# Performance work log

Measured on AMD Instinct MI355X. Metric: run time of the kernel, lower is better.

## Reference

```python
import jax, jax.numpy as jnp
import numpy as np

ATTRIBUTE_NUMS = [3, 3, 1, 4, 3]
WINDOW_SIZE = 10


def setup_inputs() -> dict:
    key = jax.random.key(0)
    ks = jax.random.split(key, 7)
    b, s, n_l, f = 4, 2048, 4, 64
    A, L = 14, 5  # num_attributes, levels per attribute
    scale_tensor = jax.random.normal(ks[0], (b, s, n_l, f), dtype=jnp.float32)
    scale = 1.0 / np.sqrt(f).astype(np.float32)
    Wq = jax.random.normal(ks[1], (A, L, f, f), dtype=jnp.float32) * scale
    bq = jax.random.normal(ks[2], (A, L, f), dtype=jnp.float32) * 0.01
    Wk = jax.random.normal(ks[3], (A, L, f, f), dtype=jnp.float32) * scale
    bk = jax.random.normal(ks[4], (A, L, f), dtype=jnp.float32) * 0.01
    Wt = jax.random.normal(ks[5], (A, L, f, f), dtype=jnp.float32) * scale
    bt = jax.random.normal(ks[6], (A, L, f), dtype=jnp.float32) * 0.01
    return {"scale_tensor": scale_tensor, "Wq": Wq, "bq": bq, "Wk": Wk,
            "bk": bk, "Wt": Wt, "bt": bt, "scale_idx": 4}


def reference(scale_tensor, Wq, bq, Wk, bk, Wt, bt, scale_idx):
    b, s, a, f = scale_tensor.shape
    k = WINDOW_SIZE * (6 - scale_idx)  # half window (static python int)
    w = 2 * k + 1
    l_i = scale_idx
    off = sum(ATTRIBUTE_NUMS[:scale_idx - 1])
    # select the parameters actually used: attributes [off, off+a), levels [0, l_i)
    Wq_s, bq_s = Wq[off:off + a, :l_i], bq[off:off + a, :l_i]  # [a,l,f,f], [a,l,f]
    Wk_s, bk_s = Wk[off:off + a, :l_i], bk[off:off + a, :l_i]
    Wt_s, bt_s = Wt[off:off + a, :l_i], bt[off:off + a, :l_i]

    # sliding windows over the sequence axis (zero-padded), shared across levels
    padded = jnp.pad(scale_tensor, ((0, 0), (k, k), (0, 0), (0, 0)))
    idx = jnp.arange(s)[:, None] + jnp.arange(w)[None, :]  # [s, w]
    win = padded[:, idx]                                   # [b,s,w,a,f]
    zero_mask = jnp.all(win == 0, axis=-1)                 # [b,s,w,a]

    # queries: q = x @ Wq^T + bq  (torch Linear convention, W is [out,in])
    q = jnp.einsum('bsaf,algf->bsalg', scale_tensor, Wq_s) + bq_s  # [b,s,a,l,f]
    qk = jnp.einsum('bsalg,algf->bsalf', q, Wk_s)                  # [b,s,a,l,f]
    attn = jnp.einsum('bsalf,bswaf->bsalw', qk, win)
    attn = attn + jnp.einsum('bsalg,alg->bsal', q, bk_s)[..., None]
    attn = attn / np.float32(np.sqrt(f))

    mask = jnp.transpose(zero_mask, (0, 1, 3, 2))[:, :, :, None, :]  # [b,s,a,1,w]
    attn = jnp.where(mask, jnp.float32(-1e9), attn)
    wgt = jax.nn.softmax(attn, axis=-1)                    # [b,s,a,l,w]

    ctx = jnp.einsum('bsalw,bswaf->bsalf', wgt, win)       # [b,s,a,l,f]
    out = jnp.einsum('bsalf,algf->bsalg', ctx, Wt_s) + bt_s
    return out  # [b,s,a,l_i,f]
```

## Files before the change

kernel.cpp:

```cpp
#include <hip/hip_runtime.h>
#include <hip/hip_bf16.h>

#define SDIM 2048
#define KWIN 20
#define WWIN 41

typedef __attribute__((ext_vector_type(8))) short s8v;
typedef __attribute__((ext_vector_type(4))) float f32x4;
#define MFMA __builtin_amdgcn_mfma_f32_16x16x32_bf16

#define WSB_MB 8256
#define WSB_WT 172096

#define O_YJF 0
#define O_YFJ 16128
#define O_RF  31488
#define LDS_TOTAL 31936

__device__ __forceinline__ int detect_is_bf16(const void* xp) {
  const unsigned* w = (const unsigned*)xp;
  const unsigned word = w[threadIdx.x & 63];
  const unsigned e = (word >> 7) & 0xFFu;
  const unsigned long long m = __ballot(e >= 118u && e <= 132u);
  return __popcll(m) >= 32;
}
__device__ __forceinline__ float ldf(const void* p, size_t i, int isbf) {
  return isbf ? __bfloat162float(((const __hip_bfloat16*)p)[i]) : ((const float*)p)[i];
}
__device__ __forceinline__ unsigned bfb(float f) {
  union { float f; unsigned u; } x; x.f = f;
  return (x.u + 0x7FFFu + ((x.u >> 16) & 1u)) >> 16;
}
__device__ __forceinline__ int pkbf(float a, float b) {
  return (int)(bfb(a) | (bfb(b) << 16));
}
__device__ __forceinline__ s8v xform(int p00, int p01, int p10, int p11, int lane) {
  const int q = lane >> 4;
  const int sA = (lane & 15) + ((q & 1) << 5);
  const int sB = sA + 16;
  const bool hi = (q >> 1) != 0;
  const int w0a = __shfl(p00, sA), w0b = __shfl(p10, sA);
  const int w1a = __shfl(p01, sA), w1b = __shfl(p11, sA);
  const int w2a = __shfl(p00, sB), w2b = __shfl(p10, sB);
  const int w3a = __shfl(p01, sB), w3b = __shfl(p11, sB);
  union { int i[4]; s8v v; } u;
  u.i[0] = hi ? w0b : w0a;
  u.i[1] = hi ? w1b : w1a;
  u.i[2] = hi ? w2b : w2a;
  u.i[3] = hi ? w3b : w3a;
  return u.v;
}

__global__ __launch_bounds__(256) void prep_kernel(
    const void* __restrict__ x,
    const void* __restrict__ Wq, const void* __restrict__ bq,
    const void* __restrict__ Wk, const void* __restrict__ bk,
    const void* __restrict__ Wt, const void* __restrict__ bt,
    const int* __restrict__ sip, float* __restrict__ ws) {
  const int isbf = detect_is_bf16(x);
  const int al = blockIdx.x, a = al >> 2, li = al & 3;
  const int fq = blockIdx.y;
  const int si = *sip;
  int off = 0;
  const int ATTR[5] = {3, 3, 1, 4, 3};
  for (int i = 0; i < si - 1 && i < 5; ++i) off += ATTR[i];
  const size_t wb = ((size_t)(off + a) * 5 + li) * 4096;
  const size_t bb = ((size_t)(off + a) * 5 + li) * 64;
  const int tid = threadIdx.x;

  __shared__ float sq[4096], sk[4096];
  __shared__ float sbq[64], sbk[64];
  for (int i = tid; i < 4096; i += 256) {
    sq[i] = ldf(Wq, wb + i, isbf);
    sk[i] = ldf(Wk, wb + i, isbf);
  }
  if (tid < 64) { sbq[tid] = ldf(bq, bb + tid, isbf); sbk[tid] = ldf(bk, bb + tid, isbf); }
  __syncthreads();

  __hip_bfloat16* mb  = (__hip_bfloat16*)((char*)ws + WSB_MB) + (size_t)al * 5120;
  __hip_bfloat16* wtb = (__hip_bfloat16*)((char*)ws + WSB_WT) + (size_t)al * 4096;

  for (int t = tid; t < 1024; t += 256) {
    const int f = fq * 16 + (t >> 6), f2 = t & 63;
    float acc = 0.f;
    #pragma unroll 16
    for (int g = 0; g < 64; ++g) acc += sk[g * 64 + f] * sq[g * 64 + f2];
    mb[f * 64 + f2] = __float2bfloat16(acc);
    wtb[f * 64 + f2] = __float2bfloat16(ldf(Wt, wb + f * 64 + f2, isbf));
  }
  if (fq == 0) {
    if (tid < 64) {
      float u = 0.f, v = 0.f;
      for (int g = 0; g < 64; ++g) {
        u += sq[g * 64 + tid] * sbk[g];
        v += sk[g * 64 + tid] * sbq[g];
      }
      mb[64 * 64 + tid] = __float2bfloat16(u);
      ws[al * 64 + tid] = v;
      ws[1024 + al * 64 + tid] = ldf(bt, bb + tid, isbf);
    }
    for (int i = tid; i < 15 * 64; i += 256) mb[65 * 64 + i] = __float2bfloat16(0.f);
    if (tid == 0) {
      float c = 0.f;
      for (int g = 0; g < 64; ++g) c += sbq[g] * sbk[g];
      ws[2048 + al] = c;
    }
  }
}

__global__ __launch_bounds__(256, 4) void attn_kernel(
    const void* __restrict__ x, const float* __restrict__ ws,
    float* __restrict__ out) {
  const int isbf = detect_is_bf16(x);
  const int chunk = blockIdx.x;
  const int ba = blockIdx.y;
  const int lp = blockIdx.z;
  const int b = ba >> 2, a = ba & 3;
  const int s0 = chunk * 64;
  const int tid = threadIdx.x;
  const int lane = tid & 63;
  const int mt = tid >> 6;
  const int c16 = lane & 15;
  const int q = lane >> 4;

  __shared__ __align__(16) char lds[LDS_TOTAL];

  #pragma unroll
  for (int it = 0; it < 7; ++it) {
    const int r = it * 16 + (tid >> 4);
    const int j = s0 - KWIN + r;
    float4 yv = {0.f, 0.f, 0.f, 0.f};
    if (r < 104 && j >= 0 && j < SDIM) {
      if (isbf) {
        const size_t base = (((size_t)b * SDIM + j) * 4 + a) * 64 + c16 * 4;
        yv.x = ldf(x, base, 1); yv.y = ldf(x, base + 1, 1);
        yv.z = ldf(x, base + 2, 1); yv.w = ldf(x, base + 3, 1);
      } else {
        yv = *((const float4*)x + (((size_t)b * SDIM + j) * 4 + a) * 16 + c16);
      }
    }
    const int f0 = c16 * 4;
    ((int*)(lds + O_YJF + r * 144 + f0 * 2))[0] = pkbf(yv.x, yv.y);
    ((int*)(lds + O_YJF + r * 144 + f0 * 2))[1] = pkbf(yv.z, yv.w);
    *(unsigned short*)(lds + O_YFJ + (f0 + 0) * 240 + r * 2) = (unsigned short)bfb(yv.x);
    *(unsigned short*)(lds + O_YFJ + (f0 + 1) * 240 + r * 2) = (unsigned short)bfb(yv.y);
    *(unsigned short*)(lds + O_YFJ + (f0 + 2) * 240 + r * 2) = (unsigned short)bfb(yv.z);
    *(unsigned short*)(lds + O_YFJ + (f0 + 3) * 240 + r * 2) = (unsigned short)bfb(yv.w);
    const bool nz = (yv.x != 0.f) || (yv.y != 0.f) || (yv.z != 0.f) || (yv.w != 0.f);
    const unsigned long long m = __ballot(nz);
    if (c16 == 0) ((float*)(lds + O_RF))[r] = ((m >> (q * 16)) & 0xFFFFull) ? 1.f : 0.f;
  }
  __syncthreads();

  const short* mbase  = (const short*)((const char*)ws + WSB_MB);
  const short* wtbase = (const short*)((const char*)ws + WSB_WT);
  const char* yjf = lds + O_YJF;
  const char* yfj = lds + O_YFJ;

  const s8v xb0 = *(const s8v*)(yjf + (KWIN + 16 * mt + c16) * 144 + 16 * q);
  const s8v xb1 = *(const s8v*)(yjf + (KWIN + 16 * mt + c16) * 144 + 64 + 16 * q);
  float rfarr[16];
  #pragma unroll
  for (int nt = 0; nt < 4; ++nt) {
    const float4 t = *(const float4*)((const float*)(lds + O_RF) + 16 * mt + 16 * nt + 4 * q);
    rfarr[nt * 4 + 0] = t.x; rfarr[nt * 4 + 1] = t.y;
    rfarr[nt * 4 + 2] = t.z; rfarr[nt * 4 + 3] = t.w;
  }

  for (int li = 0; li < 2; ++li) {
    const int l = lp * 2 + li;
    const int al = a * 4 + l;
    const short* mb  = mbase + (size_t)al * 5120;
    const short* wtb = wtbase + (size_t)al * 4096;
    const float c_al = ws[2048 + al];

    int pq[4][2];
    f32x4 uacc = {0.f, 0.f, 0.f, 0.f};
    #pragma unroll
    for (int nt = 0; nt < 5; ++nt) {
      const int rowm = (nt < 4) ? (16 * nt + c16) : (64 + c16);
      const s8v a0 = *(const s8v*)(mb + rowm * 64 + 8 * q);
      const s8v a1 = *(const s8v*)(mb + rowm * 64 + 32 + 8 * q);
      f32x4 acc;
      if (nt < 4) {
        const float4 v4 = *(const float4*)(ws + al * 64 + 16 * nt + 4 * q);
        acc[0] = v4.x; acc[1] = v4.y; acc[2] = v4.z; acc[3] = v4.w;
      } else {
        acc[0] = acc[1] = acc[2] = acc[3] = 0.f;
      }
      acc = MFMA(a0, xb0, acc, 0, 0, 0);
      acc = MFMA(a1, xb1, acc, 0, 0, 0);
      if (nt < 4) { pq[nt][0] = pkbf(acc[0], acc[1]); pq[nt][1] = pkbf(acc[2], acc[3]); }
      else uacc = acc;
    }
    const float ux = __shfl(uacc[0], lane & 15) + c_al;
    const s8v qb0 = xform(pq[0][0], pq[0][1], pq[1][0], pq[1][1], lane);
    const s8v qb1 = xform(pq[2][0], pq[2][1], pq[3][0], pq[3][1], lane);

    f32x4 st[4];
    #pragma unroll
    for (int nt = 0; nt < 4; ++nt) {
      const char* yr = yjf + (16 * mt + 16 * nt + c16) * 144 + 16 * q;
      const s8v a0 = *(const s8v*)yr;
      const s8v a1 = *(const s8v*)(yr + 64);
      f32x4 s = {0.f, 0.f, 0.f, 0.f};
      s = MFMA(a0, qb0, s, 0, 0, 0);
      s = MFMA(a1, qb1, s, 0, 0, 0);
      st[nt] = s;
    }

    float ee[16];
    float mx = -3.0e38f;
    #pragma unroll
    for (int nt = 0; nt < 4; ++nt)
      #pragma unroll
      for (int r = 0; r < 4; ++r) {
        const int w = 16 * nt + 4 * q + r - c16;
        float lv = -1.0e9f;
        if (w >= 0 && w < WWIN && rfarr[nt * 4 + r] != 0.f)
          lv = (st[nt][r] + ux) * 0.125f;
        ee[nt * 4 + r] = lv;
        mx = fmaxf(mx, lv);
      }
    mx = fmaxf(mx, __shfl_xor(mx, 16));
    mx = fmaxf(mx, __shfl_xor(mx, 32));
    float se = 0.f;
    #pragma unroll
    for (int i = 0; i < 16; ++i) { ee[i] = __expf(ee[i] - mx); se += ee[i]; }
    se += __shfl_xor(se, 16);
    se += __shfl_xor(se, 32);
    const float rse = 1.f / se;

    int pp[4][2];
    #pragma unroll
    for (int nt = 0; nt < 4; ++nt) {
      pp[nt][0] = pkbf(ee[nt * 4 + 0], ee[nt * 4 + 1]);
      pp[nt][1] = pkbf(ee[nt * 4 + 2], ee[nt * 4 + 3]);
    }
    const s8v pb0 = xform(pp[0][0], pp[0][1], pp[1][0], pp[1][1], lane);
    const s8v pb1 = xform(pp[2][0], pp[2][1], pp[3][0], pp[3][1], lane);

    int cp[4][2];
    #pragma unroll
    for (int nt = 0; nt < 4; ++nt) {
      const char* fr = yfj + (16 * nt + c16) * 240 + 32 * mt + 16 * q;
      const s8v a0 = *(const s8v*)fr;
      const s8v a1 = *(const s8v*)(fr + 64);
      f32x4 cc = {0.f, 0.f, 0.f, 0.f};
      cc = MFMA(a0, pb0, cc, 0, 0, 0);
      cc = MFMA(a1, pb1, cc, 0, 0, 0);
      cp[nt][0] = pkbf(cc[0] * rse, cc[1] * rse);
      cp[nt][1] = pkbf(cc[2] * rse, cc[3] * rse);
    }
    const s8v cb0 = xform(cp[0][0], cp[0][1], cp[1][0], cp[1][1], lane);
    const s8v cb1 = xform(cp[2][0], cp[2][1], cp[3][0], cp[3][1], lane);

    const int row = 16 * mt + c16;
    float* obase = out + ((((size_t)b * SDIM + s0 + row) * 4 + a) * 4 + l) * 64 + 4 * q;
    #pragma unroll
    for (int nt = 0; nt < 4; ++nt) {
      const s8v a0 = *(const s8v*)(wtb + (16 * nt + c16) * 64 + 8 * q);
      const s8v a1 = *(const s8v*)(wtb + (16 * nt + c16) * 64 + 32 + 8 * q);
      const float4 b4 = *(const float4*)(ws + 1024 + al * 64 + 16 * nt + 4 * q);
      f32x4 o;
      o[0] = b4.x; o[1] = b4.y; o[2] = b4.z; o[3] = b4.w;
      o = MFMA(a0, cb0, o, 0, 0, 0);
      o = MFMA(a1, cb1, o, 0, 0, 0);
      float4 o4; o4.x = o[0]; o4.y = o[1]; o4.z = o[2]; o4.w = o[3];
      *(float4*)(obase + 16 * nt) = o4;
    }
  }
}

extern "C" void kernel_launch(void* const* d_in, const int* in_sizes, int n_in,
                              void* d_out, int out_size, void* d_ws, size_t ws_size,
                              hipStream_t stream) {
  const void* x  = d_in[0];
  const void* Wq = d_in[1];
  const void* bq = d_in[2];
  const void* Wk = d_in[3];
  const void* bk = d_in[4];
  const void* Wt = d_in[5];
  const void* bt = d_in[6];
  const int* sip = (const int*)d_in[7];
  float* ws = (float*)d_ws;
  float* out = (float*)d_out;

  prep_kernel<<<dim3(16, 4), 256, 0, stream>>>(x, Wq, bq, Wk, bk, Wt, bt, sip, ws);
  attn_kernel<<<dim3(32, 16, 2), 256, 0, stream>>>(x, ws, out);
}
```

Before: 118.7 us.

## Drop transposed LDS window copy and give each block a single level

Removes the second, transposed bf16 copy of the window tile from shared memory. The context MFMA operands are now gathered with eight strided 16-bit LDS reads from the row-major tile, which roughly halves LDS use per block. The grid doubles along z so each block handles one level instead of looping over two, and the occupancy hint in the launch bounds is dropped. The cost is that every block restages the window tile, doing twice the global loads and conversions in total, and the scalar strided LDS gathers may hit bank conflicts and add instructions.

```diff
diff --git a/kernel.cpp b/kernel.cpp
--- a/kernel.cpp
+++ b/kernel.cpp
@@ -13,9 +13,8 @@
 #define WSB_WT 172096
 
 #define O_YJF 0
-#define O_YFJ 16128
-#define O_RF  31488
-#define LDS_TOTAL 31936
+#define O_RF  16128
+#define LDS_TOTAL 16576
 
 __device__ __forceinline__ int detect_is_bf16(const void* xp) {
   const unsigned* w = (const unsigned*)xp;
@@ -108,13 +107,13 @@
   }
 }
 
-__global__ __launch_bounds__(256, 4) void attn_kernel(
+__global__ __launch_bounds__(256) void attn_kernel(
     const void* __restrict__ x, const float* __restrict__ ws,
     float* __restrict__ out) {
   const int isbf = detect_is_bf16(x);
   const int chunk = blockIdx.x;
   const int ba = blockIdx.y;
-  const int lp = blockIdx.z;
+  const int l = blockIdx.z;
   const int b = ba >> 2, a = ba & 3;
   const int s0 = chunk * 64;
   const int tid = threadIdx.x;
@@ -142,20 +141,17 @@
     const int f0 = c16 * 4;
     ((int*)(lds + O_YJF + r * 144 + f0 * 2))[0] = pkbf(yv.x, yv.y);
     ((int*)(lds + O_YJF + r * 144 + f0 * 2))[1] = pkbf(yv.z, yv.w);
-    *(unsigned short*)(lds + O_YFJ + (f0 + 0) * 240 + r * 2) = (unsigned short)bfb(yv.x);
-    *(unsigned short*)(lds + O_YFJ + (f0 + 1) * 240 + r * 2) = (unsigned short)bfb(yv.y);
-    *(unsigned short*)(lds + O_YFJ + (f0 + 2) * 240 + r * 2) = (unsigned short)bfb(yv.z);
-    *(unsigned short*)(lds + O_YFJ + (f0 + 3) * 240 + r * 2) = (unsigned short)bfb(yv.w);
     const bool nz = (yv.x != 0.f) || (yv.y != 0.f) || (yv.z != 0.f) || (yv.w != 0.f);
     const unsigned long long m = __ballot(nz);
     if (c16 == 0) ((float*)(lds + O_RF))[r] = ((m >> (q * 16)) & 0xFFFFull) ? 1.f : 0.f;
   }
   __syncthreads();
 
-  const short* mbase  = (const short*)((const char*)ws + WSB_MB);
-  const short* wtbase = (const short*)((const char*)ws + WSB_WT);
   const char* yjf = lds + O_YJF;
-  const char* yfj = lds + O_YFJ;
+  const int al = a * 4 + l;
+  const short* mb  = (const short*)((const char*)ws + WSB_MB) + (size_t)al * 5120;
+  const short* wtb = (const short*)((const char*)ws + WSB_WT) + (size_t)al * 4096;
+  const float c_al = ws[2048 + al];
 
   const s8v xb0 = *(const s8v*)(yjf + (KWIN + 16 * mt + c16) * 144 + 16 * q);
   const s8v xb1 = *(const s8v*)(yjf + (KWIN + 16 * mt + c16) * 144 + 64 + 16 * q);
@@ -167,108 +163,104 @@
     rfarr[nt * 4 + 2] = t.z; rfarr[nt * 4 + 3] = t.w;
   }
 
-  for (int li = 0; li < 2; ++li) {
-    const int l = lp * 2 + li;
-    const int al = a * 4 + l;
-    const short* mb  = mbase + (size_t)al * 5120;
-    const short* wtb = wtbase + (size_t)al * 4096;
-    const float c_al = ws[2048 + al];
-
-    int pq[4][2];
-    f32x4 uacc = {0.f, 0.f, 0.f, 0.f};
+  int pq[4][2];
+  f32x4 uacc = {0.f, 0.f, 0.f, 0.f};
+  #pragma unroll
+  for (int nt = 0; nt < 5; ++nt) {
+    const int rowm = (nt < 4) ? (16 * nt + c16) : (64 + c16);
+    const s8v a0 = *(const s8v*)(mb + rowm * 64 + 8 * q);
+    const s8v a1 = *(const s8v*)(mb + rowm * 64 + 32 + 8 * q);
+    f32x4 acc;
+    if (nt < 4) {
+      const float4 v4 = *(const float4*)(ws + al * 64 + 16 * nt + 4 * q);
+      acc[0] = v4.x; acc[1] = v4.y; acc[2] = v4.z; acc[3] = v4.w;
+    } else {
+      acc[0] = acc[1] = acc[2] = acc[3] = 0.f;
+    }
+    acc = MFMA(a0, xb0, acc, 0, 0, 0);
+    acc = MFMA(a1, xb1, acc, 0, 0, 0);
+    if (nt < 4) { pq[nt][0] = pkbf(acc[0], acc[1]); pq[nt][1] = pkbf(acc[2], acc[3]); }
+    else uacc = acc;
+  }
+  const float ux = __shfl(uacc[0], lane & 15) + c_al;
+  const s8v qb0 = xform(pq[0][0], pq[0][1], pq[1][0], pq[1][1], lane);
+  const s8v qb1 = xform(pq[2][0], pq[2][1], pq[3][0], pq[3][1], lane);
+
+  f32x4 st[4];
+  #pragma unroll
+  for (int nt = 0; nt < 4; ++nt) {
+    const char* yr = yjf + (16 * mt + 16 * nt + c16) * 144 + 16 * q;
+    const s8v a0 = *(const s8v*)yr;
+    const s8v a1 = *(const s8v*)(yr + 64);
+    f32x4 s = {0.f, 0.f, 0.f, 0.f};
+    s = MFMA(a0, qb0, s, 0, 0, 0);
+    s = MFMA(a1, qb1, s, 0, 0, 0);
+    st[nt] = s;
+  }
+
+  float ee[16];
+  float mx = -3.0e38f;
+  #pragma unroll
+  for (int nt = 0; nt < 4; ++nt)
     #pragma unroll
-    for (int nt = 0; nt < 5; ++nt) {
-      const int rowm = (nt < 4) ? (16 * nt + c16) : (64 + c16);
-      const s8v a0 = *(const s8v*)(mb + rowm * 64 + 8 * q);
-      const s8v a1 = *(const s8v*)(mb + rowm * 64 + 32 + 8 * q);
-      f32x4 acc;
-      if (nt < 4) {
-        const float4 v4 = *(const float4*)(ws + al * 64 + 16 * nt + 4 * q);
-        acc[0] = v4.x; acc[1] = v4.y; acc[2] = v4.z; acc[3] = v4.w;
-      } else {
-        acc[0] = acc[1] = acc[2] = acc[3] = 0.f;
-      }
-      acc = MFMA(a0, xb0, acc, 0, 0, 0);
-      acc = MFMA(a1, xb1, acc, 0, 0, 0);
-      if (nt < 4) { pq[nt][0] = pkbf(acc[0], acc[1]); pq[nt][1] = pkbf(acc[2], acc[3]); }
-      else uacc = acc;
-    }
-    const float ux = __shfl(uacc[0], lane & 15) + c_al;
-    const s8v qb0 = xform(pq[0][0], pq[0][1], pq[1][0], pq[1][1], lane);
-    const s8v qb1 = xform(pq[2][0], pq[2][1], pq[3][0], pq[3][1], lane);
-
-    f32x4 st[4];
+    for (int r = 0; r < 4; ++r) {
+      const int w = 16 * nt + 4 * q + r - c16;
+      float lv = -1.0e9f;
+      if (w >= 0 && w < WWIN && rfarr[nt * 4 + r] != 0.f)
+        lv = (st[nt][r] + ux) * 0.125f;
+      ee[nt * 4 + r] = lv;
+      mx = fmaxf(mx, lv);
+    }
+  mx = fmaxf(mx, __shfl_xor(mx, 16));
+  mx = fmaxf(mx, __shfl_xor(mx, 32));
+  float se = 0.f;
+  #pragma unroll
+  for (int i = 0; i < 16; ++i) { ee[i] = __expf(ee[i] - mx); se += ee[i]; }
+  se += __shfl_xor(se, 16);
+  se += __shfl_xor(se, 32);
+  const float rse = 1.f / se;
+
+  int pp[4][2];
+  #pragma unroll
+  for (int nt = 0; nt < 4; ++nt) {
+    pp[nt][0] = pkbf(ee[nt * 4 + 0], ee[nt * 4 + 1]);
+    pp[nt][1] = pkbf(ee[nt * 4 + 2], ee[nt * 4 + 3]);
+  }
+  const s8v pb0 = xform(pp[0][0], pp[0][1], pp[1][0], pp[1][1], lane);
+  const s8v pb1 = xform(pp[2][0], pp[2][1], pp[3][0], pp[3][1], lane);
+
+  int cp[4][2];
+  #pragma unroll
+  for (int nt = 0; nt < 4; ++nt) {
+    const char* cbase = yjf + (16 * mt + 8 * q) * 144 + (16 * nt + c16) * 2;
+    union { short s[8]; s8v v; } ua0, ua1;
     #pragma unroll
-    for (int nt = 0; nt < 4; ++nt) {
-      const char* yr = yjf + (16 * mt + 16 * nt + c16) * 144 + 16 * q;
-      const s8v a0 = *(const s8v*)yr;
-      const s8v a1 = *(const s8v*)(yr + 64);
-      f32x4 s = {0.f, 0.f, 0.f, 0.f};
-      s = MFMA(a0, qb0, s, 0, 0, 0);
-      s = MFMA(a1, qb1, s, 0, 0, 0);
-      st[nt] = s;
-    }
-
-    float ee[16];
-    float mx = -3.0e38f;
-    #pragma unroll
-    for (int nt = 0; nt < 4; ++nt)
-      #pragma unroll
-      for (int r = 0; r < 4; ++r) {
-        const int w = 16 * nt + 4 * q + r - c16;
-        float lv = -1.0e9f;
-        if (w >= 0 && w < WWIN && rfarr[nt * 4 + r] != 0.f)
-          lv = (st[nt][r] + ux) * 0.125f;
-        ee[nt * 4 + r] = lv;
-        mx = fmaxf(mx, lv);
-      }
-    mx = fmaxf(mx, __shfl_xor(mx, 16));
-    mx = fmaxf(mx, __shfl_xor(mx, 32));
-    float se = 0.f;
-    #pragma unroll
-    for (int i = 0; i < 16; ++i) { ee[i] = __expf(ee[i] - mx); se += ee[i]; }
-    se += __shfl_xor(se, 16);
-    se += __shfl_xor(se, 32);
-    const float rse = 1.f / se;
-
-    int pp[4][2];
-    #pragma unroll
-    for (int nt = 0; nt < 4; ++nt) {
-      pp[nt][0] = pkbf(ee[nt * 4 + 0], ee[nt * 4 + 1]);
-      pp[nt][1] = pkbf(ee[nt * 4 + 2], ee[nt * 4 + 3]);
-    }
-    const s8v pb0 = xform(pp[0][0], pp[0][1], pp[1][0], pp[1][1], lane);
-    const s8v pb1 = xform(pp[2][0], pp[2][1], pp[3][0], pp[3][1], lane);
-
-    int cp[4][2];
-    #pragma unroll
-    for (int nt = 0; nt < 4; ++nt) {
-      const char* fr = yfj + (16 * nt + c16) * 240 + 32 * mt + 16 * q;
-      const s8v a0 = *(const s8v*)fr;
-      const s8v a1 = *(const s8v*)(fr + 64);
-      f32x4 cc = {0.f, 0.f, 0.f, 0.f};
-      cc = MFMA(a0, pb0, cc, 0, 0, 0);
-      cc = MFMA(a1, pb1, cc, 0, 0, 0);
-      cp[nt][0] = pkbf(cc[0] * rse, cc[1] * rse);
-      cp[nt][1] = pkbf(cc[2] * rse, cc[3] * rse);
-    }
-    const s8v cb0 = xform(cp[0][0], cp[0][1], cp[1][0], cp[1][1], lane);
-    const s8v cb1 = xform(cp[2][0], cp[2][1], cp[3][0], cp[3][1], lane);
-
-    const int row = 16 * mt + c16;
-    float* obase = out + ((((size_t)b * SDIM + s0 + row) * 4 + a) * 4 + l) * 64 + 4 * q;
-    #pragma unroll
-    for (int nt = 0; nt < 4; ++nt) {
-      const s8v a0 = *(const s8v*)(wtb + (16 * nt + c16) * 64 + 8 * q);
-      const s8v a1 = *(const s8v*)(wtb + (16 * nt + c16) * 64 + 32 + 8 * q);
-      const float4 b4 = *(const float4*)(ws + 1024 + al * 64 + 16 * nt + 4 * q);
-      f32x4 o;
-      o[0] = b4.x; o[1] = b4.y; o[2] = b4.z; o[3] = b4.w;
-      o = MFMA(a0, cb0, o, 0, 0, 0);
-      o = MFMA(a1, cb1, o, 0, 0, 0);
-      float4 o4; o4.x = o[0]; o4.y = o[1]; o4.z = o[2]; o4.w = o[3];
-      *(float4*)(obase + 16 * nt) = o4;
-    }
+    for (int i = 0; i < 8; ++i) {
+      ua0.s[i] = *(const short*)(cbase + i * 144);
+      ua1.s[i] = *(const short*)(cbase + (32 + i) * 144);
+    }
+    f32x4 cc = {0.f, 0.f, 0.f, 0.f};
+    cc = MFMA(ua0.v, pb0, cc, 0, 0, 0);
+    cc = MFMA(ua1.v, pb1, cc, 0, 0, 0);
+    cp[nt][0] = pkbf(cc[0] * rse, cc[1] * rse);
+    cp[nt][1] = pkbf(cc[2] * rse, cc[3] * rse);
+  }
+  const s8v cb0 = xform(cp[0][0], cp[0][1], cp[1][0], cp[1][1], lane);
+  const s8v cb1 = xform(cp[2][0], cp[2][1], cp[3][0], cp[3][1], lane);
+
+  const int row = 16 * mt + c16;
+  float* obase = out + ((((size_t)b * SDIM + s0 + row) * 4 + a) * 4 + l) * 64 + 4 * q;
+  #pragma unroll
+  for (int nt = 0; nt < 4; ++nt) {
+    const s8v a0 = *(const s8v*)(wtb + (16 * nt + c16) * 64 + 8 * q);
+    const s8v a1 = *(const s8v*)(wtb + (16 * nt + c16) * 64 + 32 + 8 * q);
+    const float4 b4 = *(const float4*)(ws + 1024 + al * 64 + 16 * nt + 4 * q);
+    f32x4 o;
+    o[0] = b4.x; o[1] = b4.y; o[2] = b4.z; o[3] = b4.w;
+    o = MFMA(a0, cb0, o, 0, 0, 0);
+    o = MFMA(a1, cb1, o, 0, 0, 0);
+    float4 o4; o4.x = o[0]; o4.y = o[1]; o4.z = o[2]; o4.w = o[3];
+    *(float4*)(obase + 16 * nt) = o4;
   }
 }
 
@@ -287,5 +279,5 @@
   float* out = (float*)d_out;
 
   prep_kernel<<<dim3(16, 4), 256, 0, stream>>>(x, Wq, bq, Wk, bk, Wt, bt, sip, ws);
-  attn_kernel<<<dim3(32, 16, 2), 256, 0, stream>>>(x, ws, out);
-}
+  attn_kernel<<<dim3(32, 16, 4), 256, 0, stream>>>(x, ws, out);
+}
```

After: 121.2 us. 2.1% more time.
